# Performance work log

Measured on AMD Instinct MI355X. Metric: run time of the kernel, lower is better.

The kernel has to match this reference:

```python
import jax, jax.numpy as jnp
import numpy as np

B, S, DIM_IN, DIM_K, DIM_V = 8, 4096, 1024, 128, 128


def setup_inputs() -> dict:
    key = jax.random.key(0)
    ks = jax.random.split(key, 9)
    s_in = 1.0 / np.sqrt(DIM_IN)
    return {
        "query": jax.random.normal(ks[0], (B, S, DIM_IN), jnp.float32),
        "key": jax.random.normal(ks[1], (B, S, DIM_IN), jnp.float32),
        "value": jax.random.normal(ks[2], (B, S, DIM_IN), jnp.float32),
        # Linear params stored as [in, out] (torch weight transposed)
        "Wq": jax.random.uniform(ks[3], (DIM_IN, DIM_K), jnp.float32, -s_in, s_in),
        "bq": jax.random.uniform(ks[4], (DIM_K,), jnp.float32, -s_in, s_in),
        "Wk": jax.random.uniform(ks[5], (DIM_IN, DIM_K), jnp.float32, -s_in, s_in),
        "bk": jax.random.uniform(ks[6], (DIM_K,), jnp.float32, -s_in, s_in),
        "Wv": jax.random.uniform(ks[7], (DIM_IN, DIM_V), jnp.float32, -s_in, s_in),
        "bv": jax.random.uniform(ks[8], (DIM_V,), jnp.float32, -s_in, s_in),
    }


def reference(query, key, value, Wq, bq, Wk, bk, Wv, bv):
    q = jnp.einsum("bsd,dk->bsk", query, Wq) + bq   # [B,S,DIM_K]
    k = jnp.einsum("bsd,dk->bsk", key, Wk) + bk     # [B,S,DIM_K]
    v = jnp.einsum("bsd,dv->bsv", value, Wv) + bv   # [B,S,DIM_V]
    scale = 1.0 / jnp.sqrt(jnp.asarray(q.shape[-1], q.dtype))
    scores = jnp.einsum("bqk,bsk->bqs", q, k) * scale  # [B,S,S]
    attn = jax.nn.softmax(scores, axis=-1)
    return jnp.einsum("bqs,bsv->bqv", attn, v)  # [B,S,DIM_V]
```

## Files before the change

### kernel.cpp

```cpp
#include <hip/hip_runtime.h>
#include <hip/hip_bf16.h>

typedef __attribute__((ext_vector_type(8))) short short8;
typedef __attribute__((ext_vector_type(4))) float f32x4;
typedef __attribute__((ext_vector_type(16))) float f32x16;
typedef __attribute__((ext_vector_type(4))) unsigned int u32x4;

#define MFMA16(A, B, C) __builtin_amdgcn_mfma_f32_16x16x32_bf16((A), (B), (C), 0, 0, 0)
#define MFMA32(A, B, C) __builtin_amdgcn_mfma_f32_32x32x16_bf16((A), (B), (C), 0, 0, 0)

__device__ __forceinline__ short f2bf(float x) {
  unsigned u = __float_as_uint(x);
  return (short)((u + 0x7FFFu + ((u >> 16) & 1u)) >> 16);
}

__device__ __forceinline__ unsigned cvtpk(float lo, float hi) {
  unsigned r;
  asm("v_cvt_pk_bf16_f32 %0, %1, %2" : "=v"(r) : "v"(lo), "v"(hi));
  return r;
}

__device__ __forceinline__ void gload16(const void* g, const void* s) {
  __builtin_amdgcn_global_load_lds(
      (const __attribute__((address_space(1))) unsigned int*)g,
      (__attribute__((address_space(3))) unsigned int*)s, 16, 0, 0);
}

__global__ __launch_bounds__(256) void wt_kernel(
    const float* __restrict__ Wq, const float* __restrict__ Wk, const float* __restrict__ Wv,
    short* __restrict__ WqT, short* __restrict__ WkT, short* __restrict__ WvT)
{
  const float* W  = (blockIdx.y == 0) ? Wq  : (blockIdx.y == 1) ? Wk  : Wv;
  short*       WT = (blockIdx.y == 0) ? WqT : (blockIdx.y == 1) ? WkT : WvT;
  int idx = blockIdx.x * 256 + threadIdx.x;
  int n = idx >> 10, k = idx & 1023;
  WT[idx] = f2bf(W[k * 128 + n]);
}

__global__ __launch_bounds__(256) void proj_kernel(
    const float* __restrict__ Aq, const float* __restrict__ Ak, const float* __restrict__ Av,
    const short* __restrict__ WqT, const short* __restrict__ WkT, const short* __restrict__ WvT,
    const float* __restrict__ bq, const float* __restrict__ bk, const float* __restrict__ bv,
    short* __restrict__ Qs, short* __restrict__ Ks, short* __restrict__ VTs,
    float scale_q)
{
  __shared__ short Alds[64 * 40];
  __shared__ short Wlds[128 * 40];
  const int y = blockIdx.y;
  const float* A    = (y == 0) ? Aq  : (y == 1) ? Ak  : Av;
  const short* WT   = (y == 0) ? WqT : (y == 1) ? WkT : WvT;
  const float* bias = (y == 0) ? bq  : (y == 1) ? bk  : bv;
  const int tid = threadIdx.x;
  const int lane = tid & 63, w = tid >> 6;
  const int g = (lane >> 4) & 3, ql = lane & 15;
  const long m0 = (long)blockIdx.x * 64;

  const f32x4 fzero = {0.f, 0.f, 0.f, 0.f};
  f32x4 acc[8];
  #pragma unroll
  for (int i = 0; i < 8; ++i) acc[i] = fzero;

  const int arow = tid >> 2, ac0 = (tid & 3) * 8;
  const int wn1 = (w >> 1) * 64, wm1 = (w & 1) * 32;
  const int wn2 = w * 32;

  for (int kk = 0; kk < 1024; kk += 32) {
    __syncthreads();
    {
      const float* src = A + (m0 + arow) * 1024 + kk + ac0;
      float4 a0 = *(const float4*)(src);
      float4 a1 = *(const float4*)(src + 4);
      short8 pb;
      pb[0] = f2bf(a0.x); pb[1] = f2bf(a0.y); pb[2] = f2bf(a0.z); pb[3] = f2bf(a0.w);
      pb[4] = f2bf(a1.x); pb[5] = f2bf(a1.y); pb[6] = f2bf(a1.z); pb[7] = f2bf(a1.w);
      *(short8*)&Alds[arow * 40 + ac0] = pb;
    }
    #pragma unroll
    for (int cc = 0; cc < 2; ++cc) {
      int c = tid + cc * 256;
      int n = c >> 2, i0 = (c & 3) * 8;
      *(short8*)&Wlds[n * 40 + i0] = *(const short8*)(WT + n * 1024 + kk + i0);
    }
    __syncthreads();
    if (y < 2) {
      short8 af[2], bf[4];
      #pragma unroll
      for (int mt = 0; mt < 2; ++mt)
        af[mt] = *(const short8*)&Alds[(wm1 + 16 * mt + ql) * 40 + g * 8];
      #pragma unroll
      for (int nt = 0; nt < 4; ++nt)
        bf[nt] = *(const short8*)&Wlds[(wn1 + 16 * nt + ql) * 40 + g * 8];
      #pragma unroll
      for (int mt = 0; mt < 2; ++mt)
        #pragma unroll
        for (int nt = 0; nt < 4; ++nt)
          acc[mt * 4 + nt] = MFMA16(af[mt], bf[nt], acc[mt * 4 + nt]);
    } else {
      short8 af[2], bf[4];
      #pragma unroll
      for (int nt = 0; nt < 2; ++nt)
        af[nt] = *(const short8*)&Wlds[(wn2 + 16 * nt + ql) * 40 + g * 8];
      #pragma unroll
      for (int mt = 0; mt < 4; ++mt)
        bf[mt] = *(const short8*)&Alds[(16 * mt + ql) * 40 + g * 8];
      #pragma unroll
      for (int nt = 0; nt < 2; ++nt)
        #pragma unroll
        for (int mt = 0; mt < 4; ++mt)
          acc[nt * 4 + mt] = MFMA16(af[nt], bf[mt], acc[nt * 4 + mt]);
    }
  }

  if (y < 2) {
    short* Out = (y == 0) ? Qs : Ks;
    const float sc = (y == 0) ? scale_q : 1.0f;
    #pragma unroll
    for (int nt = 0; nt < 4; ++nt) {
      int n = wn1 + 16 * nt + ql;
      float bs = bias[n];
      #pragma unroll
      for (int mt = 0; mt < 2; ++mt)
        #pragma unroll
        for (int r = 0; r < 4; ++r) {
          long m = m0 + wm1 + 16 * mt + 4 * g + r;
          Out[m * 128 + n] = f2bf((acc[mt * 4 + nt][r] + bs) * sc);
        }
    }
  } else {
    #pragma unroll
    for (int nt = 0; nt < 2; ++nt)
      #pragma unroll
      for (int r = 0; r < 4; ++r) {
        int n = wn2 + 16 * nt + 4 * g + r;
        float bs = bias[n];
        #pragma unroll
        for (int mt = 0; mt < 4; ++mt) {
          long m = m0 + 16 * mt + ql;
          VTs[(long)n * 32768 + m] = f2bf(acc[nt * 4 + mt][r] + bs);
        }
      }
  }
}

__global__ __launch_bounds__(256, 2) void attn_kernel(
    const short* __restrict__ Q,
    const short* __restrict__ K,
    const short* __restrict__ VT,
    float* __restrict__ O0,
    float* __restrict__ O1,
    float2* __restrict__ stats,
    int ntiles)
{
  __shared__ short lds[32768];
  const int tid = threadIdx.x, l = tid & 63, w = tid >> 6;
  const int l31 = l & 31, hi = l >> 5, xm = (l & 7) << 3;
  const int qb = blockIdx.x, h = blockIdx.y;
  const int b = qb >> 5;
  const int qrow = qb * 128 + w * 32 + l31;
  const long kv0 = (long)b * 4096 + (long)h * ntiles * 64;

  short8 qf[8];
  const short* Qp = Q + (long)qrow * 128 + hi * 8;
  #pragma unroll
  for (int ds = 0; ds < 8; ++ds) qf[ds] = *(const short8*)(Qp + ds * 16);

  const short* Kt = K + kv0 * 128;
  const short* Vt = VT + kv0;
  int kg_off[4]; long vg_off[4];
  #pragma unroll
  for (int r = 0; r < 4; ++r) {
    int c = r * 256 + tid;
    int p = c * 16;
    kg_off[r] = (p ^ (((p >> 8) & 7) << 4)) >> 1;
    int e = (p ^ (((p >> 7) & 7) << 4)) >> 1;
    vg_off[r] = (long)(e >> 6) * 32768 + (e & 63);
  }

  #define STAGE(bb, t) { \
    const short* kg_ = Kt + (t) * 8192; \
    const short* vg_ = Vt + (t) * 64; \
    _Pragma("unroll") \
    for (int r = 0; r < 4; ++r) { \
      gload16(kg_ + kg_off[r], &lds[(bb) * 16384 + r * 2048 + w * 512]); \
      gload16(vg_ + vg_off[r], &lds[(bb) * 16384 + 8192 + r * 2048 + w * 512]); \
    } }

  f32x16 acc0 = {}, acc1 = {}, acc2 = {}, acc3 = {};
  float m = -3e38f, lsum = 0.f;
  const int kread = l31 * 128;

  STAGE(0, 0);

  for (int t = 0; t < ntiles; ++t) {
    const int bb = t & 1;
    if (t + 1 < ntiles) {
      STAGE(bb ^ 1, t + 1);
      asm volatile("s_waitcnt vmcnt(8)" ::: "memory");
    } else {
      asm volatile("s_waitcnt vmcnt(0)" ::: "memory");
    }
    __builtin_amdgcn_s_barrier();

    const short* kb = &lds[bb * 16384];
    const short* vb = &lds[bb * 16384 + 8192];

    f32x16 st0 = {}, st1 = {};
    #pragma unroll
    for (int ds = 0; ds < 8; ++ds) {
      int co = (ds * 16 + hi * 8) ^ xm;
      short8 kf0 = *(const short8*)(kb + kread + co);
      short8 kf1 = *(const short8*)(kb + 4096 + kread + co);
      st0 = MFMA32(kf0, qf[ds], st0);
      st1 = MFMA32(kf1, qf[ds], st1);
    }

    float a0 = fmaxf(fmaxf(st0[0], st0[1]),  fmaxf(st0[2], st0[3]));
    float a1 = fmaxf(fmaxf(st0[4], st0[5]),  fmaxf(st0[6], st0[7]));
    float a2 = fmaxf(fmaxf(st0[8], st0[9]),  fmaxf(st0[10], st0[11]));
    float a3 = fmaxf(fmaxf(st0[12], st0[13]), fmaxf(st0[14], st0[15]));
    float b0 = fmaxf(fmaxf(st1[0], st1[1]),  fmaxf(st1[2], st1[3]));
    float b1 = fmaxf(fmaxf(st1[4], st1[5]),  fmaxf(st1[6], st1[7]));
    float b2 = fmaxf(fmaxf(st1[8], st1[9]),  fmaxf(st1[10], st1[11]));
    float b3 = fmaxf(fmaxf(st1[12], st1[13]), fmaxf(st1[14], st1[15]));
    float pm = fmaxf(fmaxf(fmaxf(a0, a1), fmaxf(a2, a3)),
                     fmaxf(fmaxf(b0, b1), fmaxf(b2, b3)));
    pm = fmaxf(pm, __shfl_xor(pm, 32));
    if (!__all(pm <= m + 8.f)) {
      float mn = fmaxf(m, pm);
      float al = exp2f(m - mn);
      m = mn;
      lsum *= al;
      acc0 *= al; acc1 *= al; acc2 *= al; acc3 *= al;
    }
    float ts = 0.f;
    #pragma unroll
    for (int j = 0; j < 16; ++j) { st0[j] = exp2f(st0[j] - m); ts += st0[j]; }
    #pragma unroll
    for (int j = 0; j < 16; ++j) { st1[j] = exp2f(st1[j] - m); ts += st1[j]; }
    ts += __shfl_xor(ts, 32);
    lsum += ts;

    unsigned pk[16];
    #pragma unroll
    for (int j = 0; j < 8; ++j) pk[j]     = cvtpk(st0[2 * j], st0[2 * j + 1]);
    #pragma unroll
    for (int j = 0; j < 8; ++j) pk[8 + j] = cvtpk(st1[2 * j], st1[2 * j + 1]);

    #pragma unroll
    for (int f = 0; f < 4; ++f) {
      auto r02 = __builtin_amdgcn_permlane32_swap(pk[f * 4 + 0], pk[f * 4 + 2], false, false);
      auto r13 = __builtin_amdgcn_permlane32_swap(pk[f * 4 + 1], pk[f * 4 + 3], false, false);
      union { u32x4 u; short8 s; } pf;
      pf.u = (u32x4){r02[0], r13[0], r02[1], r13[1]};
      int vo = (f * 16 + hi * 8) ^ xm;
      acc0 = MFMA32(*(const short8*)(vb +        l31 * 64 + vo), pf.s, acc0);
      acc1 = MFMA32(*(const short8*)(vb + 2048 + l31 * 64 + vo), pf.s, acc1);
      acc2 = MFMA32(*(const short8*)(vb + 4096 + l31 * 64 + vo), pf.s, acc2);
      acc3 = MFMA32(*(const short8*)(vb + 6144 + l31 * 64 + vo), pf.s, acc3);
    }

    asm volatile("s_waitcnt lgkmcnt(0)" ::: "memory");
    __builtin_amdgcn_s_barrier();
  }

  float* Op = ((h == 0) ? O0 : O1) + (long)qrow * 128;
  #define STORE_DT(A, dtb) { \
    _Pragma("unroll") \
    for (int jj = 0; jj < 4; ++jj) { \
      f32x4 o_ = {A[4 * jj], A[4 * jj + 1], A[4 * jj + 2], A[4 * jj + 3]}; \
      *(f32x4*)(Op + (dtb) + jj * 8 + hi * 4) = o_; \
    } }
  STORE_DT(acc0, 0) STORE_DT(acc1, 32) STORE_DT(acc2, 64) STORE_DT(acc3, 96)

  if (l < 32) stats[(long)h * 32768 + qrow] = make_float2(m, lsum);
}

__global__ __launch_bounds__(256) void merge_kernel(
    float* __restrict__ O, const float* __restrict__ O1,
    const float2* __restrict__ stats, int halves)
{
  int idx = blockIdx.x * 256 + threadIdx.x;
  int q = idx >> 5, c = (idx & 31) * 4;
  long off = (long)q * 128 + c;
  float2 s0 = stats[q];
  f32x4 a = *(const f32x4*)(O + off);
  if (halves == 2) {
    float2 s1 = stats[32768 + q];
    float M = fmaxf(s0.x, s1.x);
    float w0 = exp2f(s0.x - M), w1 = exp2f(s1.x - M);
    f32x4 bv = *(const f32x4*)(O1 + off);
    float inv = 1.f / (w0 * s0.y + w1 * s1.y);
    a = (a * w0 + bv * w1) * inv;
  } else {
    a = a * (1.f / s0.y);
  }
  *(f32x4*)(O + off) = a;
}

extern "C" void kernel_launch(void* const* d_in, const int* in_sizes, int n_in,
                              void* d_out, int out_size, void* d_ws, size_t ws_size,
                              hipStream_t stream) {
  const float* query = (const float*)d_in[0];
  const float* key   = (const float*)d_in[1];
  const float* value = (const float*)d_in[2];
  const float* Wq = (const float*)d_in[3];
  const float* bq = (const float*)d_in[4];
  const float* Wk = (const float*)d_in[5];
  const float* bk = (const float*)d_in[6];
  const float* Wv = (const float*)d_in[7];
  const float* bv = (const float*)d_in[8];

  char* wsb = (char*)d_ws;
  short* Qs  = (short*)(wsb);
  short* Ks  = (short*)(wsb + 8388608);
  short* VTs = (short*)(wsb + 16777216);
  short* WqT = (short*)(wsb + 25165824);
  short* WkT = (short*)(wsb + 25427968);
  short* WvT = (short*)(wsb + 25690112);
  float* O1  = (float*)(wsb + 25952256);
  const size_t NEED2 = 25952256ull + 16777216ull + 524288ull;
  int halves = (ws_size >= NEED2) ? 2 : 1;
  float2* stats = (float2*)(wsb + (halves == 2 ? 42729472ull : 25952256ull));
  int ntiles = (halves == 2) ? 32 : 64;

  wt_kernel<<<dim3(512, 3), 256, 0, stream>>>(Wq, Wk, Wv, WqT, WkT, WvT);
  const float scale_q = 0.08838834764831845f * 1.4426950408889634f;
  proj_kernel<<<dim3(512, 3), 256, 0, stream>>>(query, key, value, WqT, WkT, WvT,
                                                bq, bk, bv, Qs, Ks, VTs, scale_q);
  attn_kernel<<<dim3(256, halves), 256, 0, stream>>>(Qs, Ks, VTs, (float*)d_out, O1, stats, ntiles);
  merge_kernel<<<4096, 256, 0, stream>>>((float*)d_out, O1, stats, halves);
}
```

Baseline: 226.7 us.

## Rewrite projection GEMM as LDS-free per-wave 32x32 MFMA with direct global loads

The projection kernel drops its shared-memory staging and barriers. Each wave now computes a 32-row by 128-column tile with four 32x32x16 bf16 MFMAs, loading activations and transposed weights straight from global memory into registers. The grid is halved and launch bounds ask for three blocks per CU. This removes LDS traffic and syncthreads, but each wave re-reads the whole weight matrix from cache with no sharing across the block, and the output stores are narrow scattered writes.

```diff
diff --git a/kernel.cpp b/kernel.cpp
--- a/kernel.cpp
+++ b/kernel.cpp
@@ -37,108 +37,78 @@
   WT[idx] = f2bf(W[k * 128 + n]);
 }
 
-__global__ __launch_bounds__(256) void proj_kernel(
+__global__ __launch_bounds__(256, 3) void proj_kernel(
     const float* __restrict__ Aq, const float* __restrict__ Ak, const float* __restrict__ Av,
     const short* __restrict__ WqT, const short* __restrict__ WkT, const short* __restrict__ WvT,
     const float* __restrict__ bq, const float* __restrict__ bk, const float* __restrict__ bv,
     short* __restrict__ Qs, short* __restrict__ Ks, short* __restrict__ VTs,
     float scale_q)
 {
-  __shared__ short Alds[64 * 40];
-  __shared__ short Wlds[128 * 40];
   const int y = blockIdx.y;
   const float* A    = (y == 0) ? Aq  : (y == 1) ? Ak  : Av;
   const short* WT   = (y == 0) ? WqT : (y == 1) ? WkT : WvT;
   const float* bias = (y == 0) ? bq  : (y == 1) ? bk  : bv;
-  const int tid = threadIdx.x;
-  const int lane = tid & 63, w = tid >> 6;
-  const int g = (lane >> 4) & 3, ql = lane & 15;
-  const long m0 = (long)blockIdx.x * 64;
-
-  const f32x4 fzero = {0.f, 0.f, 0.f, 0.f};
-  f32x4 acc[8];
-  #pragma unroll
-  for (int i = 0; i < 8; ++i) acc[i] = fzero;
-
-  const int arow = tid >> 2, ac0 = (tid & 3) * 8;
-  const int wn1 = (w >> 1) * 64, wm1 = (w & 1) * 32;
-  const int wn2 = w * 32;
-
-  for (int kk = 0; kk < 1024; kk += 32) {
-    __syncthreads();
-    {
-      const float* src = A + (m0 + arow) * 1024 + kk + ac0;
-      float4 a0 = *(const float4*)(src);
-      float4 a1 = *(const float4*)(src + 4);
-      short8 pb;
-      pb[0] = f2bf(a0.x); pb[1] = f2bf(a0.y); pb[2] = f2bf(a0.z); pb[3] = f2bf(a0.w);
-      pb[4] = f2bf(a1.x); pb[5] = f2bf(a1.y); pb[6] = f2bf(a1.z); pb[7] = f2bf(a1.w);
-      *(short8*)&Alds[arow * 40 + ac0] = pb;
-    }
-    #pragma unroll
-    for (int cc = 0; cc < 2; ++cc) {
-      int c = tid + cc * 256;
-      int n = c >> 2, i0 = (c & 3) * 8;
-      *(short8*)&Wlds[n * 40 + i0] = *(const short8*)(WT + n * 1024 + kk + i0);
-    }
-    __syncthreads();
-    if (y < 2) {
-      short8 af[2], bf[4];
-      #pragma unroll
-      for (int mt = 0; mt < 2; ++mt)
-        af[mt] = *(const short8*)&Alds[(wm1 + 16 * mt + ql) * 40 + g * 8];
-      #pragma unroll
-      for (int nt = 0; nt < 4; ++nt)
-        bf[nt] = *(const short8*)&Wlds[(wn1 + 16 * nt + ql) * 40 + g * 8];
-      #pragma unroll
-      for (int mt = 0; mt < 2; ++mt)
-        #pragma unroll
-        for (int nt = 0; nt < 4; ++nt)
-          acc[mt * 4 + nt] = MFMA16(af[mt], bf[nt], acc[mt * 4 + nt]);
-    } else {
-      short8 af[2], bf[4];
-      #pragma unroll
-      for (int nt = 0; nt < 2; ++nt)
-        af[nt] = *(const short8*)&Wlds[(wn2 + 16 * nt + ql) * 40 + g * 8];
-      #pragma unroll
-      for (int mt = 0; mt < 4; ++mt)
-        bf[mt] = *(const short8*)&Alds[(16 * mt + ql) * 40 + g * 8];
-      #pragma unroll
-      for (int nt = 0; nt < 2; ++nt)
-        #pragma unroll
-        for (int mt = 0; mt < 4; ++mt)
-          acc[nt * 4 + mt] = MFMA16(af[nt], bf[mt], acc[nt * 4 + mt]);
-    }
-  }
+  const int tid = threadIdx.x, l = tid & 63, w = tid >> 6;
+  const int l31 = l & 31, hi = l >> 5;
+  const long m0 = (long)(blockIdx.x * 4 + w) * 32;
+
+  const float* Ap = A + (m0 + l31) * 1024 + hi * 8;
+  const short* Wp = WT + (long)l31 * 1024 + hi * 8;
+
+  f32x16 acc0 = {}, acc1 = {}, acc2 = {}, acc3 = {};
 
   if (y < 2) {
+    #pragma unroll 2
+    for (int kk = 0; kk < 1024; kk += 16) {
+      float4 a0 = *(const float4*)(Ap + kk);
+      float4 a1 = *(const float4*)(Ap + kk + 4);
+      short8 w0 = *(const short8*)(Wp + kk);
+      short8 w1 = *(const short8*)(Wp + 32768 + kk);
+      short8 w2 = *(const short8*)(Wp + 65536 + kk);
+      short8 w3 = *(const short8*)(Wp + 98304 + kk);
+      short8 af;
+      af[0] = f2bf(a0.x); af[1] = f2bf(a0.y); af[2] = f2bf(a0.z); af[3] = f2bf(a0.w);
+      af[4] = f2bf(a1.x); af[5] = f2bf(a1.y); af[6] = f2bf(a1.z); af[7] = f2bf(a1.w);
+      acc0 = MFMA32(af, w0, acc0);
+      acc1 = MFMA32(af, w1, acc1);
+      acc2 = MFMA32(af, w2, acc2);
+      acc3 = MFMA32(af, w3, acc3);
+    }
     short* Out = (y == 0) ? Qs : Ks;
     const float sc = (y == 0) ? scale_q : 1.0f;
-    #pragma unroll
-    for (int nt = 0; nt < 4; ++nt) {
-      int n = wn1 + 16 * nt + ql;
-      float bs = bias[n];
-      #pragma unroll
-      for (int mt = 0; mt < 2; ++mt)
-        #pragma unroll
-        for (int r = 0; r < 4; ++r) {
-          long m = m0 + wm1 + 16 * mt + 4 * g + r;
-          Out[m * 128 + n] = f2bf((acc[mt * 4 + nt][r] + bs) * sc);
-        }
-    }
+#define STORE_QK(A_, nt) { \
+    const int n_ = (nt) * 32 + l31; \
+    const float bs_ = bias[n_]; \
+    _Pragma("unroll") \
+    for (int r = 0; r < 16; ++r) { \
+      const int row_ = (r & 3) + 8 * (r >> 2) + 4 * hi; \
+      Out[(m0 + row_) * 128 + n_] = f2bf((A_[r] + bs_) * sc); \
+    } }
+    STORE_QK(acc0, 0) STORE_QK(acc1, 1) STORE_QK(acc2, 2) STORE_QK(acc3, 3)
   } else {
-    #pragma unroll
-    for (int nt = 0; nt < 2; ++nt)
-      #pragma unroll
-      for (int r = 0; r < 4; ++r) {
-        int n = wn2 + 16 * nt + 4 * g + r;
-        float bs = bias[n];
-        #pragma unroll
-        for (int mt = 0; mt < 4; ++mt) {
-          long m = m0 + 16 * mt + ql;
-          VTs[(long)n * 32768 + m] = f2bf(acc[nt * 4 + mt][r] + bs);
-        }
-      }
+    #pragma unroll 2
+    for (int kk = 0; kk < 1024; kk += 16) {
+      float4 a0 = *(const float4*)(Ap + kk);
+      float4 a1 = *(const float4*)(Ap + kk + 4);
+      short8 w0 = *(const short8*)(Wp + kk);
+      short8 w1 = *(const short8*)(Wp + 32768 + kk);
+      short8 w2 = *(const short8*)(Wp + 65536 + kk);
+      short8 w3 = *(const short8*)(Wp + 98304 + kk);
+      short8 af;
+      af[0] = f2bf(a0.x); af[1] = f2bf(a0.y); af[2] = f2bf(a0.z); af[3] = f2bf(a0.w);
+      af[4] = f2bf(a1.x); af[5] = f2bf(a1.y); af[6] = f2bf(a1.z); af[7] = f2bf(a1.w);
+      acc0 = MFMA32(w0, af, acc0);
+      acc1 = MFMA32(w1, af, acc1);
+      acc2 = MFMA32(w2, af, acc2);
+      acc3 = MFMA32(w3, af, acc3);
+    }
+#define STORE_V(A_, dt) { \
+    _Pragma("unroll") \
+    for (int r = 0; r < 16; ++r) { \
+      const int dv_ = (dt) * 32 + (r & 3) + 8 * (r >> 2) + 4 * hi; \
+      VTs[(long)dv_ * 32768 + m0 + l31] = f2bf(A_[r] + bias[dv_]); \
+    } }
+    STORE_V(acc0, 0) STORE_V(acc1, 1) STORE_V(acc2, 2) STORE_V(acc3, 3)
   }
 }
 
@@ -325,7 +295,7 @@
 
   wt_kernel<<<dim3(512, 3), 256, 0, stream>>>(Wq, Wk, Wv, WqT, WkT, WvT);
   const float scale_q = 0.08838834764831845f * 1.4426950408889634f;
-  proj_kernel<<<dim3(512, 3), 256, 0, stream>>>(query, key, value, WqT, WkT, WvT,
+  proj_kernel<<<dim3(256, 3), 256, 0, stream>>>(query, key, value, WqT, WkT, WvT,
                                                 bq, bk, bv, Qs, Ks, VTs, scale_q);
   attn_kernel<<<dim3(256, halves), 256, 0, stream>>>(Qs, Ks, VTs, (float*)d_out, O1, stats, ntiles);
   merge_kernel<<<4096, 256, 0, stream>>>((float*)d_out, O1, stats, halves);
```

Result: slower. 288.0 us (+27.1%).
